# Kernel optimization log

Measured on AMD Instinct MI355X. Metric: run time of the kernel, lower is better.

Reference implementation:

```python
import jax, jax.numpy as jnp
import numpy as np

N, E, D, K = 32768, 16384, 4, 8          # nodes, hyperedges, edges/node, nodes/edge
IN_DIM, OUT_DIM, EDGE_DIM, NUM_HEADS = 128, 128, 64, 8


def setup_inputs() -> dict:
    key = jax.random.key(0)
    ks = jax.random.split(key, 16)
    s_in = 1.0 / np.sqrt(IN_DIM)
    s_out = 1.0 / np.sqrt(OUT_DIM)
    s_edge = 1.0 / np.sqrt(EDGE_DIM)
    return {
        "x": jax.random.normal(ks[0], (N, IN_DIM), jnp.float32),
        "edge_attr": jax.random.normal(ks[1], (E, EDGE_DIM), jnp.float32),
        "node_edges": jax.random.randint(ks[2], (N, D), 0, E),   # hyperedges containing each node
        "edge_nodes": jax.random.randint(ks[3], (E, K), 0, N),   # nodes inside each hyperedge
        "W_lin": jax.random.normal(ks[4], (OUT_DIM, IN_DIM), jnp.float32) * s_in,
        "W_edge": jax.random.normal(ks[5], (OUT_DIM, EDGE_DIM), jnp.float32) * s_edge,
        "Wq": jax.random.normal(ks[6], (OUT_DIM, OUT_DIM), jnp.float32) * s_out,
        "Wk": jax.random.normal(ks[7], (OUT_DIM, OUT_DIM), jnp.float32) * s_out,
        "Wv": jax.random.normal(ks[8], (OUT_DIM, OUT_DIM), jnp.float32) * s_out,
        "bq": jnp.zeros((OUT_DIM,), jnp.float32),
        "bk": jnp.zeros((OUT_DIM,), jnp.float32),
        "bv": jnp.zeros((OUT_DIM,), jnp.float32),
        "Wo": jax.random.normal(ks[9], (OUT_DIM, OUT_DIM), jnp.float32) * s_out,
        "bo": jnp.zeros((OUT_DIM,), jnp.float32),
    }


def reference(x, edge_attr, node_edges, edge_nodes,
              W_lin, W_edge, Wq, Wk, Wv, bq, bk, bv, Wo, bo):
    n, out_dim = x.shape[0], W_lin.shape[0]
    hd = out_dim // NUM_HEADS
    L = node_edges.shape[1] * edge_nodes.shape[1]  # D*K keys per node

    Wh = x @ W_lin.T                               # [N, out]
    We = edge_attr @ W_edge.T                      # [E, out]

    u_idx = edge_nodes[node_edges]                 # [N, D, K] neighbor node ids
    vals = Wh[u_idx]                               # [N, D, K, out]
    keys = vals + We[node_edges][:, :, None, :]    # key = Wh[u] + We[e]
    keys = keys.reshape(n, L, out_dim)
    vals = vals.reshape(n, L, out_dim)

    # torch nn.MultiheadAttention: single query per node (query = Wh[v])
    q = (Wh @ Wq.T + bq).reshape(n, NUM_HEADS, hd)
    k = (keys @ Wk.T + bk).reshape(n, L, NUM_HEADS, hd)
    v = (vals @ Wv.T + bv).reshape(n, L, NUM_HEADS, hd)

    scores = jnp.einsum('nhd,nlhd->nhl', q, k) / jnp.sqrt(jnp.asarray(hd, q.dtype))
    attn = jax.nn.softmax(scores, axis=-1)         # [N, H, L]
    ctx = jnp.einsum('nhl,nlhd->nhd', attn, v).reshape(n, out_dim)
    out = ctx @ Wo.T + bo
    return jax.nn.relu(out)
```

## Files before the change

### kernel.cpp

```cpp
#include <hip/hip_runtime.h>

#define N_NODES 32768
#define N_EDGES 16384
#define DEG 4
#define KPE 8
#define DIM 128
#define EDIM 64

typedef float f32x4 __attribute__((ext_vector_type(4)));
typedef __bf16 bf16x8 __attribute__((ext_vector_type(8)));
typedef __bf16 bf16x2 __attribute__((ext_vector_type(2)));
typedef unsigned short u16x8 __attribute__((ext_vector_type(8)));

static __device__ __forceinline__ unsigned short f2bf(float f) {
  union { float f; unsigned int u; } v; v.f = f;
  unsigned int r = (v.u + 0x7FFFu + ((v.u >> 16) & 1u)) >> 16;
  return (unsigned short)r;
}
static __device__ __forceinline__ float bflo(unsigned int v) {
  union { unsigned int u; float f; } x; x.u = v << 16; return x.f;
}
static __device__ __forceinline__ float bfhi(unsigned int v) {
  union { unsigned int u; float f; } x; x.u = v & 0xffff0000u; return x.f;
}

#if __has_builtin(__builtin_amdgcn_fdot2_f32_bf16)
static __device__ __forceinline__ float dot2bf(unsigned int a, unsigned int b, float c) {
  return __builtin_amdgcn_fdot2_f32_bf16(
      __builtin_bit_cast(bf16x2, a), __builtin_bit_cast(bf16x2, b), c, false);
}
#else
static __device__ __forceinline__ float dot2bf(unsigned int a, unsigned int b, float c) {
  c = fmaf(bflo(a), bflo(b), c);
  return fmaf(bfhi(a), bfhi(b), c);
}
#endif

__global__ __launch_bounds__(256) void wprep_kernel(
    const float* __restrict__ Wq, const float* __restrict__ Wk,
    const float* __restrict__ Wv, const float* __restrict__ Wlin,
    const float* __restrict__ Wedge, const float* __restrict__ Wo,
    unsigned short* __restrict__ CW, unsigned short* __restrict__ CWE,
    unsigned short* __restrict__ Wob)
{
  int id = blockIdx.x * 256 + threadIdx.x;
  if (id < 384 * 128) {
    int j = id >> 7, i = id & 127;
    const float* wrow; float scale = 1.0f;
    if (j < 128)      { wrow = Wq + j * 128; scale = 0.25f; }
    else if (j < 256) { wrow = Wk + (j - 128) * 128; }
    else              { wrow = Wv + (j - 256) * 128; }
    float s = 0.f;
    #pragma unroll 8
    for (int m = 0; m < 128; ++m) s += wrow[m] * Wlin[m * 128 + i];
    CW[id] = f2bf(s * scale);
  } else if (id < 384 * 128 + 128 * 64) {
    int id2 = id - 384 * 128; int j = id2 >> 6, t = id2 & 63;
    float s = 0.f;
    #pragma unroll 8
    for (int m = 0; m < 128; ++m) s += Wk[j * 128 + m] * Wedge[m * 64 + t];
    CWE[id2] = f2bf(s);
  } else if (id < 384 * 128 + 128 * 64 + 128 * 128) {
    int id3 = id - (384 * 128 + 128 * 64);
    Wob[id3] = f2bf(Wo[id3]);
  }
}

__global__ __launch_bounds__(256) void g1_kernel(
    const float* __restrict__ x, const unsigned short* __restrict__ CW,
    const float* __restrict__ bq, const float* __restrict__ bv,
    unsigned short* __restrict__ qb, unsigned short* __restrict__ Kb,
    unsigned short* __restrict__ Vb)
{
  const int wave = threadIdx.x >> 6, lane = threadIdx.x & 63;
  const int r16 = lane & 15, quad = lane >> 4;
  const int m0 = blockIdx.x * 64 + wave * 16;

  u16x8 av[4];
  const float* arow = x + (size_t)(m0 + r16) * DIM + quad * 8;
  #pragma unroll
  for (int kk = 0; kk < 4; ++kk) {
    float4 a0 = *(const float4*)(arow + kk * 32);
    float4 a1 = *(const float4*)(arow + kk * 32 + 4);
    u16x8 au;
    au[0] = f2bf(a0.x); au[1] = f2bf(a0.y); au[2] = f2bf(a0.z); au[3] = f2bf(a0.w);
    au[4] = f2bf(a1.x); au[5] = f2bf(a1.y); au[6] = f2bf(a1.z); au[7] = f2bf(a1.w);
    av[kk] = au;
  }

  #pragma unroll
  for (int g = 0; g < 6; ++g) {
    f32x4 acc[4];
    const f32x4 z = {0.f, 0.f, 0.f, 0.f};
    acc[0] = z; acc[1] = z; acc[2] = z; acc[3] = z;
    #pragma unroll
    for (int kk = 0; kk < 4; ++kk) {
      #pragma unroll
      for (int s = 0; s < 4; ++s) {
        u16x8 bu = *(const u16x8*)(CW + (size_t)(g * 64 + s * 16 + r16) * DIM + kk * 32 + quad * 8);
        acc[s] = __builtin_amdgcn_mfma_f32_16x16x32_bf16(
            __builtin_bit_cast(bf16x8, av[kk]), __builtin_bit_cast(bf16x8, bu), acc[s], 0, 0, 0);
      }
    }
    const int arr = g >> 1;
    const int colbase = (g & 1) * 64;
    unsigned short* dst = arr == 0 ? qb : (arr == 1 ? Kb : Vb);
    #pragma unroll
    for (int s = 0; s < 4; ++s) {
      int j = colbase + s * 16 + r16;
      float bias = arr == 0 ? 0.25f * bq[j] : (arr == 2 ? bv[j] : 0.f);
      #pragma unroll
      for (int r = 0; r < 4; ++r) {
        int m = m0 + quad * 4 + r;
        dst[(size_t)m * DIM + j] = f2bf(acc[s][r] + bias);
      }
    }
  }
}

__global__ __launch_bounds__(256) void g2_kernel(
    const float* __restrict__ ea, const unsigned short* __restrict__ CWE,
    const float* __restrict__ bk, unsigned short* __restrict__ WeKb)
{
  const int wave = threadIdx.x >> 6, lane = threadIdx.x & 63;
  const int r16 = lane & 15, quad = lane >> 4;
  const int m0 = blockIdx.x * 64 + wave * 16;
  const int n0 = blockIdx.y * 64;

  f32x4 acc[4];
  const f32x4 z = {0.f, 0.f, 0.f, 0.f};
  acc[0] = z; acc[1] = z; acc[2] = z; acc[3] = z;

  const float* arow = ea + (size_t)(m0 + r16) * EDIM + quad * 8;
  #pragma unroll
  for (int kk = 0; kk < 2; ++kk) {
    float4 a0 = *(const float4*)(arow + kk * 32);
    float4 a1 = *(const float4*)(arow + kk * 32 + 4);
    u16x8 au;
    au[0] = f2bf(a0.x); au[1] = f2bf(a0.y); au[2] = f2bf(a0.z); au[3] = f2bf(a0.w);
    au[4] = f2bf(a1.x); au[5] = f2bf(a1.y); au[6] = f2bf(a1.z); au[7] = f2bf(a1.w);
    bf16x8 av = __builtin_bit_cast(bf16x8, au);
    #pragma unroll
    for (int s = 0; s < 4; ++s) {
      u16x8 bu = *(const u16x8*)(CWE + (size_t)(n0 + s * 16 + r16) * EDIM + kk * 32 + quad * 8);
      acc[s] = __builtin_amdgcn_mfma_f32_16x16x32_bf16(
          av, __builtin_bit_cast(bf16x8, bu), acc[s], 0, 0, 0);
    }
  }

  #pragma unroll
  for (int s = 0; s < 4; ++s) {
    int j = n0 + s * 16 + r16;
    float bias = bk[j];
    #pragma unroll
    for (int r = 0; r < 4; ++r) {
      int m = m0 + quad * 4 + r;
      WeKb[(size_t)m * DIM + j] = f2bf(acc[s][r] + bias);
    }
  }
}

__global__ __launch_bounds__(256) void attn_kernel(
    const unsigned short* __restrict__ qb, const unsigned short* __restrict__ Kb,
    const unsigned short* __restrict__ Vb, const unsigned short* __restrict__ WeKb,
    const int* __restrict__ nedges, const int* __restrict__ enodes,
    unsigned short* __restrict__ ctxb)
{
  __shared__ __align__(16) float ldsP[4][288];
  const int wave = threadIdx.x >> 6, lane = threadIdx.x & 63;
  const int n = blockIdx.x * 4 + wave;
  const int l = lane & 31, half = lane >> 5;
  const int j = l >> 3, lo8 = l & 7;
  const int c0 = lane * 2;
  const int h = lane >> 3;

  int4 e4 = *(const int4*)(nedges + (size_t)n * DEG);
  int e = (j & 2) ? ((j & 1) ? e4.w : e4.z) : ((j & 1) ? e4.y : e4.x);
  int u = enodes[(size_t)e * KPE + lo8];

  int uu[32];
  *(int4*)&uu[0]  = *(const int4*)(enodes + (size_t)e4.x * KPE);
  *(int4*)&uu[4]  = *(const int4*)(enodes + (size_t)e4.x * KPE + 4);
  *(int4*)&uu[8]  = *(const int4*)(enodes + (size_t)e4.y * KPE);
  *(int4*)&uu[12] = *(const int4*)(enodes + (size_t)e4.y * KPE + 4);
  *(int4*)&uu[16] = *(const int4*)(enodes + (size_t)e4.z * KPE);
  *(int4*)&uu[20] = *(const int4*)(enodes + (size_t)e4.z * KPE + 4);
  *(int4*)&uu[24] = *(const int4*)(enodes + (size_t)e4.w * KPE);
  *(int4*)&uu[28] = *(const int4*)(enodes + (size_t)e4.w * KPE + 4);

  const uint4* qp = (const uint4*)(qb + (size_t)n * DIM + half * 64);
  const uint4* kp = (const uint4*)(Kb + (size_t)u * DIM + half * 64);
  const uint4* ep = (const uint4*)(WeKb + (size_t)e * DIM + half * 64);

  uint4 qv[8], kv[8], ev[8];
  #pragma unroll
  for (int ch = 0; ch < 8; ++ch) qv[ch] = qp[ch];
  #pragma unroll
  for (int ch = 0; ch < 8; ++ch) kv[ch] = kp[ch];
  #pragma unroll
  for (int ch = 0; ch < 8; ++ch) ev[ch] = ep[ch];

  unsigned int vv[32];
  #pragma unroll
  for (int t = 0; t < 32; ++t)
    vv[t] = *(const unsigned int*)(Vb + (size_t)uu[t] * DIM + c0);

  float s[4] = {0.f, 0.f, 0.f, 0.f};
  #pragma unroll
  for (int ch = 0; ch < 8; ++ch) {
    const int hi = ch >> 1;
    float t = s[hi];
    t = dot2bf(qv[ch].x, kv[ch].x, t); t = dot2bf(qv[ch].x, ev[ch].x, t);
    t = dot2bf(qv[ch].y, kv[ch].y, t); t = dot2bf(qv[ch].y, ev[ch].y, t);
    t = dot2bf(qv[ch].z, kv[ch].z, t); t = dot2bf(qv[ch].z, ev[ch].z, t);
    t = dot2bf(qv[ch].w, kv[ch].w, t); t = dot2bf(qv[ch].w, ev[ch].w, t);
    s[hi] = t;
  }

  #pragma unroll
  for (int hi = 0; hi < 4; ++hi) {
    float vmax = s[hi];
    #pragma unroll
    for (int off = 16; off >= 1; off >>= 1)
      vmax = fmaxf(vmax, __shfl_xor(vmax, off, 32));
    float ex = __expf(s[hi] - vmax);
    float sum = ex;
    #pragma unroll
    for (int off = 16; off >= 1; off >>= 1)
      sum += __shfl_xor(sum, off, 32);
    ldsP[wave][(half * 4 + hi) * 36 + l] = ex / sum;
  }
  __syncthreads();

  float a0 = 0.f, a1 = 0.f;
  #pragma unroll
  for (int t = 0; t < 8; ++t) {
    float4 p4 = *(const float4*)&ldsP[wave][h * 36 + t * 4];
    a0 = fmaf(p4.x, bflo(vv[t * 4 + 0]), a0); a1 = fmaf(p4.x, bfhi(vv[t * 4 + 0]), a1);
    a0 = fmaf(p4.y, bflo(vv[t * 4 + 1]), a0); a1 = fmaf(p4.y, bfhi(vv[t * 4 + 1]), a1);
    a0 = fmaf(p4.z, bflo(vv[t * 4 + 2]), a0); a1 = fmaf(p4.z, bfhi(vv[t * 4 + 2]), a1);
    a0 = fmaf(p4.w, bflo(vv[t * 4 + 3]), a0); a1 = fmaf(p4.w, bfhi(vv[t * 4 + 3]), a1);
  }
  unsigned int pk = (unsigned int)f2bf(a0) | ((unsigned int)f2bf(a1) << 16);
  *(unsigned int*)(ctxb + (size_t)n * DIM + c0) = pk;
}

__global__ __launch_bounds__(256) void g4_kernel(
    const unsigned short* __restrict__ ctxb, const unsigned short* __restrict__ Wob,
    const float* __restrict__ bo, float* __restrict__ out)
{
  const int wave = threadIdx.x >> 6, lane = threadIdx.x & 63;
  const int r16 = lane & 15, quad = lane >> 4;
  const int m0 = blockIdx.x * 64 + wave * 16;
  const int n0 = blockIdx.y * 64;

  f32x4 acc[4];
  const f32x4 z = {0.f, 0.f, 0.f, 0.f};
  acc[0] = z; acc[1] = z; acc[2] = z; acc[3] = z;

  #pragma unroll
  for (int kk = 0; kk < 4; ++kk) {
    u16x8 au = *(const u16x8*)(ctxb + (size_t)(m0 + r16) * DIM + kk * 32 + quad * 8);
    bf16x8 av = __builtin_bit_cast(bf16x8, au);
    #pragma unroll
    for (int s = 0; s < 4; ++s) {
      u16x8 bu = *(const u16x8*)(Wob + (size_t)(n0 + s * 16 + r16) * DIM + kk * 32 + quad * 8);
      acc[s] = __builtin_amdgcn_mfma_f32_16x16x32_bf16(
          av, __builtin_bit_cast(bf16x8, bu), acc[s], 0, 0, 0);
    }
  }

  #pragma unroll
  for (int s = 0; s < 4; ++s) {
    int j = n0 + s * 16 + r16;
    float bias = bo[j];
    #pragma unroll
    for (int r = 0; r < 4; ++r) {
      int m = m0 + quad * 4 + r;
      float v = acc[s][r] + bias;
      out[(size_t)m * DIM + j] = v > 0.f ? v : 0.f;
    }
  }
}

extern "C" void kernel_launch(void* const* d_in, const int* in_sizes, int n_in,
                              void* d_out, int out_size, void* d_ws, size_t ws_size,
                              hipStream_t stream)
{
  const float* x     = (const float*)d_in[0];
  const float* ea    = (const float*)d_in[1];
  const int* nedges  = (const int*)d_in[2];
  const int* enodes  = (const int*)d_in[3];
  const float* Wlin  = (const float*)d_in[4];
  const float* Wedge = (const float*)d_in[5];
  const float* Wq    = (const float*)d_in[6];
  const float* Wk    = (const float*)d_in[7];
  const float* Wv    = (const float*)d_in[8];
  const float* bq    = (const float*)d_in[9];
  const float* bk    = (const float*)d_in[10];
  const float* bv    = (const float*)d_in[11];
  const float* Wo    = (const float*)d_in[12];
  const float* bo    = (const float*)d_in[13];
  float* out = (float*)d_out;

  unsigned short* wsp = (unsigned short*)d_ws;
  unsigned short* CW   = wsp;  wsp += 384 * 128;
  unsigned short* CWE  = wsp;  wsp += 128 * 64;
  unsigned short* Wob  = wsp;  wsp += 128 * 128;
  unsigned short* qb   = wsp;  wsp += (size_t)N_NODES * DIM;
  unsigned short* Kb   = wsp;  wsp += (size_t)N_NODES * DIM;
  unsigned short* Vb   = wsp;  wsp += (size_t)N_NODES * DIM;
  unsigned short* WeKb = wsp;  wsp += (size_t)N_EDGES * DIM;
  unsigned short* ctxb = wsp;  wsp += (size_t)N_NODES * DIM;

  wprep_kernel<<<dim3(288), dim3(256), 0, stream>>>(Wq, Wk, Wv, Wlin, Wedge, Wo, CW, CWE, Wob);
  g1_kernel<<<dim3(512), dim3(256), 0, stream>>>(x, CW, bq, bv, qb, Kb, Vb);
  g2_kernel<<<dim3(256, 2), dim3(256), 0, stream>>>(ea, CWE, bk, WeKb);
  attn_kernel<<<dim3(8192), dim3(256), 0, stream>>>(qb, Kb, Vb, WeKb, nedges, enodes, ctxb);
  g4_kernel<<<dim3(512, 2), dim3(256), 0, stream>>>(ctxb, Wob, bo, out);
}
```

Measured before the change: 230.7 us.

## Stage V gathers into LDS via global_load_lds with one node per block

The attention kernel now launches one 64-thread block per node instead of four waves per 256-thread block. It gathers the 32 neighbour V rows directly into shared memory with global_load_lds rather than into 32 per-lane registers. The goal is to cut VGPR pressure and raise occupancy so more gather latency is hidden. In exchange it uses more LDS per block, adds many small blocks with higher launch overhead, and needs LDS reads in the weighted-sum loop.

```diff
diff --git a/kernel.cpp b/kernel.cpp
--- a/kernel.cpp
+++ b/kernel.cpp
@@ -11,6 +11,7 @@
 typedef __bf16 bf16x8 __attribute__((ext_vector_type(8)));
 typedef __bf16 bf16x2 __attribute__((ext_vector_type(2)));
 typedef unsigned short u16x8 __attribute__((ext_vector_type(8)));
+typedef unsigned int u32;
 
 static __device__ __forceinline__ unsigned short f2bf(float f) {
   union { float f; unsigned int u; } v; v.f = f;
@@ -160,15 +161,16 @@
   }
 }
 
-__global__ __launch_bounds__(256) void attn_kernel(
+__global__ __launch_bounds__(64, 2) void attn_kernel(
     const unsigned short* __restrict__ qb, const unsigned short* __restrict__ Kb,
     const unsigned short* __restrict__ Vb, const unsigned short* __restrict__ WeKb,
     const int* __restrict__ nedges, const int* __restrict__ enodes,
     unsigned short* __restrict__ ctxb)
 {
-  __shared__ __align__(16) float ldsP[4][288];
-  const int wave = threadIdx.x >> 6, lane = threadIdx.x & 63;
-  const int n = blockIdx.x * 4 + wave;
+  __shared__ __align__(16) unsigned short ldsV[32][128];
+  __shared__ __align__(16) float ldsP[8][36];
+  const int lane = threadIdx.x;
+  const int n = blockIdx.x;
   const int l = lane & 31, half = lane >> 5;
   const int j = l >> 3, lo8 = l & 7;
   const int c0 = lane * 2;
@@ -178,20 +180,18 @@
   int e = (j & 2) ? ((j & 1) ? e4.w : e4.z) : ((j & 1) ? e4.y : e4.x);
   int u = enodes[(size_t)e * KPE + lo8];
 
-  int uu[32];
-  *(int4*)&uu[0]  = *(const int4*)(enodes + (size_t)e4.x * KPE);
-  *(int4*)&uu[4]  = *(const int4*)(enodes + (size_t)e4.x * KPE + 4);
-  *(int4*)&uu[8]  = *(const int4*)(enodes + (size_t)e4.y * KPE);
-  *(int4*)&uu[12] = *(const int4*)(enodes + (size_t)e4.y * KPE + 4);
-  *(int4*)&uu[16] = *(const int4*)(enodes + (size_t)e4.z * KPE);
-  *(int4*)&uu[20] = *(const int4*)(enodes + (size_t)e4.z * KPE + 4);
-  *(int4*)&uu[24] = *(const int4*)(enodes + (size_t)e4.w * KPE);
-  *(int4*)&uu[28] = *(const int4*)(enodes + (size_t)e4.w * KPE + 4);
+  int4 m0 = *(const int4*)(enodes + (size_t)e4.x * KPE);
+  int4 m1 = *(const int4*)(enodes + (size_t)e4.x * KPE + 4);
+  int4 m2 = *(const int4*)(enodes + (size_t)e4.y * KPE);
+  int4 m3 = *(const int4*)(enodes + (size_t)e4.y * KPE + 4);
+  int4 m4 = *(const int4*)(enodes + (size_t)e4.z * KPE);
+  int4 m5 = *(const int4*)(enodes + (size_t)e4.z * KPE + 4);
+  int4 m6 = *(const int4*)(enodes + (size_t)e4.w * KPE);
+  int4 m7 = *(const int4*)(enodes + (size_t)e4.w * KPE + 4);
 
   const uint4* qp = (const uint4*)(qb + (size_t)n * DIM + half * 64);
   const uint4* kp = (const uint4*)(Kb + (size_t)u * DIM + half * 64);
   const uint4* ep = (const uint4*)(WeKb + (size_t)e * DIM + half * 64);
-
   uint4 qv[8], kv[8], ev[8];
   #pragma unroll
   for (int ch = 0; ch < 8; ++ch) qv[ch] = qp[ch];
@@ -200,10 +200,21 @@
   #pragma unroll
   for (int ch = 0; ch < 8; ++ch) ev[ch] = ep[ch];
 
-  unsigned int vv[32];
-  #pragma unroll
-  for (int t = 0; t < 32; ++t)
-    vv[t] = *(const unsigned int*)(Vb + (size_t)uu[t] * DIM + c0);
+#define STAGE_V(t, node) do {                                                   \
+    const u32* gp_ = (const u32*)(Vb + (size_t)(node) * DIM) + lane;            \
+    __builtin_amdgcn_global_load_lds(                                           \
+        (const __attribute__((address_space(1))) u32*)gp_,                      \
+        (__attribute__((address_space(3))) u32*)&ldsV[t][0], 4, 0, 0);          \
+  } while (0)
+  STAGE_V(0,  m0.x); STAGE_V(1,  m0.y); STAGE_V(2,  m0.z); STAGE_V(3,  m0.w);
+  STAGE_V(4,  m1.x); STAGE_V(5,  m1.y); STAGE_V(6,  m1.z); STAGE_V(7,  m1.w);
+  STAGE_V(8,  m2.x); STAGE_V(9,  m2.y); STAGE_V(10, m2.z); STAGE_V(11, m2.w);
+  STAGE_V(12, m3.x); STAGE_V(13, m3.y); STAGE_V(14, m3.z); STAGE_V(15, m3.w);
+  STAGE_V(16, m4.x); STAGE_V(17, m4.y); STAGE_V(18, m4.z); STAGE_V(19, m4.w);
+  STAGE_V(20, m5.x); STAGE_V(21, m5.y); STAGE_V(22, m5.z); STAGE_V(23, m5.w);
+  STAGE_V(24, m6.x); STAGE_V(25, m6.y); STAGE_V(26, m6.z); STAGE_V(27, m6.w);
+  STAGE_V(28, m7.x); STAGE_V(29, m7.y); STAGE_V(30, m7.z); STAGE_V(31, m7.w);
+#undef STAGE_V
 
   float s[4] = {0.f, 0.f, 0.f, 0.f};
   #pragma unroll
@@ -228,18 +239,22 @@
     #pragma unroll
     for (int off = 16; off >= 1; off >>= 1)
       sum += __shfl_xor(sum, off, 32);
-    ldsP[wave][(half * 4 + hi) * 36 + l] = ex / sum;
+    ldsP[half * 4 + hi][l] = ex / sum;
   }
   __syncthreads();
 
   float a0 = 0.f, a1 = 0.f;
   #pragma unroll
   for (int t = 0; t < 8; ++t) {
-    float4 p4 = *(const float4*)&ldsP[wave][h * 36 + t * 4];
-    a0 = fmaf(p4.x, bflo(vv[t * 4 + 0]), a0); a1 = fmaf(p4.x, bfhi(vv[t * 4 + 0]), a1);
-    a0 = fmaf(p4.y, bflo(vv[t * 4 + 1]), a0); a1 = fmaf(p4.y, bfhi(vv[t * 4 + 1]), a1);
-    a0 = fmaf(p4.z, bflo(vv[t * 4 + 2]), a0); a1 = fmaf(p4.z, bfhi(vv[t * 4 + 2]), a1);
-    a0 = fmaf(p4.w, bflo(vv[t * 4 + 3]), a0); a1 = fmaf(p4.w, bfhi(vv[t * 4 + 3]), a1);
+    float4 p4 = *(const float4*)&ldsP[h][t * 4];
+    u32 v0 = *(const u32*)&ldsV[t * 4 + 0][c0];
+    u32 v1 = *(const u32*)&ldsV[t * 4 + 1][c0];
+    u32 v2 = *(const u32*)&ldsV[t * 4 + 2][c0];
+    u32 v3 = *(const u32*)&ldsV[t * 4 + 3][c0];
+    a0 = fmaf(p4.x, bflo(v0), a0); a1 = fmaf(p4.x, bfhi(v0), a1);
+    a0 = fmaf(p4.y, bflo(v1), a0); a1 = fmaf(p4.y, bfhi(v1), a1);
+    a0 = fmaf(p4.z, bflo(v2), a0); a1 = fmaf(p4.z, bfhi(v2), a1);
+    a0 = fmaf(p4.w, bflo(v3), a0); a1 = fmaf(p4.w, bfhi(v3), a1);
   }
   unsigned int pk = (unsigned int)f2bf(a0) | ((unsigned int)f2bf(a1) << 16);
   *(unsigned int*)(ctxb + (size_t)n * DIM + c0) = pk;
@@ -316,6 +331,6 @@
   wprep_kernel<<<dim3(288), dim3(256), 0, stream>>>(Wq, Wk, Wv, Wlin, Wedge, Wo, CW, CWE, Wob);
   g1_kernel<<<dim3(512), dim3(256), 0, stream>>>(x, CW, bq, bv, qb, Kb, Vb);
   g2_kernel<<<dim3(256, 2), dim3(256), 0, stream>>>(ea, CWE, bk, WeKb);
-  attn_kernel<<<dim3(8192), dim3(256), 0, stream>>>(qb, Kb, Vb, WeKb, nedges, enodes, ctxb);
+  attn_kernel<<<dim3(32768), dim3(64), 0, stream>>>(qb, Kb, Vb, WeKb, nedges, enodes, ctxb);
   g4_kernel<<<dim3(512, 2), dim3(256), 0, stream>>>(ctxb, Wob, bo, out);
 }
```

Result: faster. 215.5 us (-6.6%).

## Pipeline attention gathers via global_load_lds double buffering and merge projection kernels

Applied to the files above, without the earlier changes.

The attention kernel now runs one wave per block, processing 8 nodes each, and stages each node's gathered K, V, edge-key and query rows into LDS with direct global-to-LDS loads. Buffers are double-buffered so the next node's gathers are in flight while the current node's scores and context are computed, with hand-written vmcnt waits. The node and edge projection GEMMs are merged into one launch to save a kernel launch. The hard-coded waitcnt counts are fragile and depend on how many loads the compiler emits, and the large LDS footprint limits occupancy.

```diff
diff --git a/kernel.cpp b/kernel.cpp
--- a/kernel.cpp
+++ b/kernel.cpp
@@ -11,6 +11,7 @@
 typedef __bf16 bf16x8 __attribute__((ext_vector_type(8)));
 typedef __bf16 bf16x2 __attribute__((ext_vector_type(2)));
 typedef unsigned short u16x8 __attribute__((ext_vector_type(8)));
+typedef unsigned int u32;
 
 static __device__ __forceinline__ unsigned short f2bf(float f) {
   union { float f; unsigned int u; } v; v.f = f;
@@ -66,183 +67,244 @@
   }
 }
 
-__global__ __launch_bounds__(256) void g1_kernel(
+__global__ __launch_bounds__(256) void g12_kernel(
     const float* __restrict__ x, const unsigned short* __restrict__ CW,
     const float* __restrict__ bq, const float* __restrict__ bv,
     unsigned short* __restrict__ qb, unsigned short* __restrict__ Kb,
-    unsigned short* __restrict__ Vb)
+    unsigned short* __restrict__ Vb,
+    const float* __restrict__ ea, const unsigned short* __restrict__ CWE,
+    const float* __restrict__ bk, unsigned short* __restrict__ WeKb)
 {
   const int wave = threadIdx.x >> 6, lane = threadIdx.x & 63;
   const int r16 = lane & 15, quad = lane >> 4;
-  const int m0 = blockIdx.x * 64 + wave * 16;
-
-  u16x8 av[4];
-  const float* arow = x + (size_t)(m0 + r16) * DIM + quad * 8;
-  #pragma unroll
-  for (int kk = 0; kk < 4; ++kk) {
-    float4 a0 = *(const float4*)(arow + kk * 32);
-    float4 a1 = *(const float4*)(arow + kk * 32 + 4);
-    u16x8 au;
-    au[0] = f2bf(a0.x); au[1] = f2bf(a0.y); au[2] = f2bf(a0.z); au[3] = f2bf(a0.w);
-    au[4] = f2bf(a1.x); au[5] = f2bf(a1.y); au[6] = f2bf(a1.z); au[7] = f2bf(a1.w);
-    av[kk] = au;
-  }
-
-  #pragma unroll
-  for (int g = 0; g < 6; ++g) {
+
+  if (blockIdx.x < 512) {
+    const int m0 = blockIdx.x * 64 + wave * 16;
+    u16x8 av[4];
+    const float* arow = x + (size_t)(m0 + r16) * DIM + quad * 8;
+    #pragma unroll
+    for (int kk = 0; kk < 4; ++kk) {
+      float4 a0 = *(const float4*)(arow + kk * 32);
+      float4 a1 = *(const float4*)(arow + kk * 32 + 4);
+      u16x8 au;
+      au[0] = f2bf(a0.x); au[1] = f2bf(a0.y); au[2] = f2bf(a0.z); au[3] = f2bf(a0.w);
+      au[4] = f2bf(a1.x); au[5] = f2bf(a1.y); au[6] = f2bf(a1.z); au[7] = f2bf(a1.w);
+      av[kk] = au;
+    }
+    #pragma unroll
+    for (int g = 0; g < 6; ++g) {
+      f32x4 acc[4];
+      const f32x4 z = {0.f, 0.f, 0.f, 0.f};
+      acc[0] = z; acc[1] = z; acc[2] = z; acc[3] = z;
+      #pragma unroll
+      for (int kk = 0; kk < 4; ++kk) {
+        #pragma unroll
+        for (int s = 0; s < 4; ++s) {
+          u16x8 bu = *(const u16x8*)(CW + (size_t)(g * 64 + s * 16 + r16) * DIM + kk * 32 + quad * 8);
+          acc[s] = __builtin_amdgcn_mfma_f32_16x16x32_bf16(
+              __builtin_bit_cast(bf16x8, av[kk]), __builtin_bit_cast(bf16x8, bu), acc[s], 0, 0, 0);
+        }
+      }
+      const int arr = g >> 1;
+      const int colbase = (g & 1) * 64;
+      unsigned short* dst = arr == 0 ? qb : (arr == 1 ? Kb : Vb);
+      #pragma unroll
+      for (int s = 0; s < 4; ++s) {
+        int j = colbase + s * 16 + r16;
+        float bias = arr == 0 ? 0.25f * bq[j] : (arr == 2 ? bv[j] : 0.f);
+        #pragma unroll
+        for (int r = 0; r < 4; ++r) {
+          int m = m0 + quad * 4 + r;
+          dst[(size_t)m * DIM + j] = f2bf(acc[s][r] + bias);
+        }
+      }
+    }
+  } else {
+    const int idx = blockIdx.x - 512;
+    const int m0 = (idx >> 1) * 64 + wave * 16;
+    const int n0 = (idx & 1) * 64;
     f32x4 acc[4];
     const f32x4 z = {0.f, 0.f, 0.f, 0.f};
     acc[0] = z; acc[1] = z; acc[2] = z; acc[3] = z;
-    #pragma unroll
-    for (int kk = 0; kk < 4; ++kk) {
+    const float* arow = ea + (size_t)(m0 + r16) * EDIM + quad * 8;
+    #pragma unroll
+    for (int kk = 0; kk < 2; ++kk) {
+      float4 a0 = *(const float4*)(arow + kk * 32);
+      float4 a1 = *(const float4*)(arow + kk * 32 + 4);
+      u16x8 au;
+      au[0] = f2bf(a0.x); au[1] = f2bf(a0.y); au[2] = f2bf(a0.z); au[3] = f2bf(a0.w);
+      au[4] = f2bf(a1.x); au[5] = f2bf(a1.y); au[6] = f2bf(a1.z); au[7] = f2bf(a1.w);
+      bf16x8 av = __builtin_bit_cast(bf16x8, au);
       #pragma unroll
       for (int s = 0; s < 4; ++s) {
-        u16x8 bu = *(const u16x8*)(CW + (size_t)(g * 64 + s * 16 + r16) * DIM + kk * 32 + quad * 8);
+        u16x8 bu = *(const u16x8*)(CWE + (size_t)(n0 + s * 16 + r16) * EDIM + kk * 32 + quad * 8);
         acc[s] = __builtin_amdgcn_mfma_f32_16x16x32_bf16(
-            __builtin_bit_cast(bf16x8, av[kk]), __builtin_bit_cast(bf16x8, bu), acc[s], 0, 0, 0);
+            av, __builtin_bit_cast(bf16x8, bu), acc[s], 0, 0, 0);
       }
     }
-    const int arr = g >> 1;
-    const int colbase = (g & 1) * 64;
-    unsigned short* dst = arr == 0 ? qb : (arr == 1 ? Kb : Vb);
     #pragma unroll
     for (int s = 0; s < 4; ++s) {
-      int j = colbase + s * 16 + r16;
-      float bias = arr == 0 ? 0.25f * bq[j] : (arr == 2 ? bv[j] : 0.f);
+      int j = n0 + s * 16 + r16;
+      float bias = bk[j];
       #pragma unroll
       for (int r = 0; r < 4; ++r) {
         int m = m0 + quad * 4 + r;
-        dst[(size_t)m * DIM + j] = f2bf(acc[s][r] + bias);
+        WeKb[(size_t)m * DIM + j] = f2bf(acc[s][r] + bias);
       }
     }
   }
 }
 
-__global__ __launch_bounds__(256) void g2_kernel(
-    const float* __restrict__ ea, const unsigned short* __restrict__ CWE,
-    const float* __restrict__ bk, unsigned short* __restrict__ WeKb)
-{
-  const int wave = threadIdx.x >> 6, lane = threadIdx.x & 63;
-  const int r16 = lane & 15, quad = lane >> 4;
-  const int m0 = blockIdx.x * 64 + wave * 16;
-  const int n0 = blockIdx.y * 64;
-
-  f32x4 acc[4];
-  const f32x4 z = {0.f, 0.f, 0.f, 0.f};
-  acc[0] = z; acc[1] = z; acc[2] = z; acc[3] = z;
-
-  const float* arow = ea + (size_t)(m0 + r16) * EDIM + quad * 8;
-  #pragma unroll
-  for (int kk = 0; kk < 2; ++kk) {
-    float4 a0 = *(const float4*)(arow + kk * 32);
-    float4 a1 = *(const float4*)(arow + kk * 32 + 4);
-    u16x8 au;
-    au[0] = f2bf(a0.x); au[1] = f2bf(a0.y); au[2] = f2bf(a0.z); au[3] = f2bf(a0.w);
-    au[4] = f2bf(a1.x); au[5] = f2bf(a1.y); au[6] = f2bf(a1.z); au[7] = f2bf(a1.w);
-    bf16x8 av = __builtin_bit_cast(bf16x8, au);
-    #pragma unroll
-    for (int s = 0; s < 4; ++s) {
-      u16x8 bu = *(const u16x8*)(CWE + (size_t)(n0 + s * 16 + r16) * EDIM + kk * 32 + quad * 8);
-      acc[s] = __builtin_amdgcn_mfma_f32_16x16x32_bf16(
-          av, __builtin_bit_cast(bf16x8, bu), acc[s], 0, 0, 0);
-    }
-  }
-
-  #pragma unroll
-  for (int s = 0; s < 4; ++s) {
-    int j = n0 + s * 16 + r16;
-    float bias = bk[j];
-    #pragma unroll
-    for (int r = 0; r < 4; ++r) {
-      int m = m0 + quad * 4 + r;
-      WeKb[(size_t)m * DIM + j] = f2bf(acc[s][r] + bias);
-    }
-  }
-}
-
-__global__ __launch_bounds__(256) void attn_kernel(
+#define OFF_V 0
+#define OFF_K 8192
+#define OFF_E 16896
+#define OFF_Q 17984
+#define BUFSZ 18256
+#define OFF_P 36512
+
+struct IdxPack { int4 e4, m0, m1, m2, m3, m4, m5, m6, m7; };
+
+static __device__ __forceinline__ IdxPack load_idx(
+    const int* __restrict__ ne, const int* __restrict__ en, int n) {
+  IdxPack I;
+  I.e4 = *(const int4*)(ne + (size_t)n * DEG);
+  I.m0 = *(const int4*)(en + (size_t)I.e4.x * KPE);
+  I.m1 = *(const int4*)(en + (size_t)I.e4.x * KPE + 4);
+  I.m2 = *(const int4*)(en + (size_t)I.e4.y * KPE);
+  I.m3 = *(const int4*)(en + (size_t)I.e4.y * KPE + 4);
+  I.m4 = *(const int4*)(en + (size_t)I.e4.z * KPE);
+  I.m5 = *(const int4*)(en + (size_t)I.e4.z * KPE + 4);
+  I.m6 = *(const int4*)(en + (size_t)I.e4.w * KPE);
+  I.m7 = *(const int4*)(en + (size_t)I.e4.w * KPE + 4);
+  return I;
+}
+
+#define GLDS(gp, ldsp, sz) __builtin_amdgcn_global_load_lds(               \
+    (const __attribute__((address_space(1))) u32*)(gp),                    \
+    (__attribute__((address_space(3))) u32*)(ldsp), sz, 0, 0)
+
+static __device__ __forceinline__ void stage_node(
+    unsigned char* buf, const IdxPack& I,
+    const unsigned short* __restrict__ Kb, const unsigned short* __restrict__ Vb,
+    const unsigned short* __restrict__ WeKb, const unsigned short* __restrict__ qb,
+    int n, int lane)
+{
+  int4 mm[8] = {I.m0, I.m1, I.m2, I.m3, I.m4, I.m5, I.m6, I.m7};
+  #pragma unroll
+  for (int t = 0; t < 8; ++t) {
+    GLDS((const u32*)(Kb + (size_t)mm[t].x * DIM) + lane, buf + OFF_K + (t*4+0)*272, 4);
+    GLDS((const u32*)(Kb + (size_t)mm[t].y * DIM) + lane, buf + OFF_K + (t*4+1)*272, 4);
+    GLDS((const u32*)(Kb + (size_t)mm[t].z * DIM) + lane, buf + OFF_K + (t*4+2)*272, 4);
+    GLDS((const u32*)(Kb + (size_t)mm[t].w * DIM) + lane, buf + OFF_K + (t*4+3)*272, 4);
+  }
+  GLDS((const u32*)(WeKb + (size_t)I.e4.x * DIM) + lane, buf + OFF_E + 0*272, 4);
+  GLDS((const u32*)(WeKb + (size_t)I.e4.y * DIM) + lane, buf + OFF_E + 1*272, 4);
+  GLDS((const u32*)(WeKb + (size_t)I.e4.z * DIM) + lane, buf + OFF_E + 2*272, 4);
+  GLDS((const u32*)(WeKb + (size_t)I.e4.w * DIM) + lane, buf + OFF_E + 3*272, 4);
+  GLDS((const u32*)(qb + (size_t)n * DIM) + lane, buf + OFF_Q, 4);
+  const int vr = lane >> 4, vc = lane & 15;
+  #pragma unroll
+  for (int t = 0; t < 8; ++t) {
+    int row = (vr & 2) ? ((vr & 1) ? mm[t].w : mm[t].z)
+                       : ((vr & 1) ? mm[t].y : mm[t].x);
+    GLDS((const u32*)(Vb + (size_t)row * DIM) + vc * 4, buf + OFF_V + t * 1024, 16);
+  }
+}
+
+static __device__ __forceinline__ void scores_softmax(
+    const unsigned char* buf, float* ldsP, int lane)
+{
+  const int l = lane & 31, half = lane >> 5;
+  const unsigned char* krow = buf + OFF_K + l * 272 + half * 128;
+  const unsigned char* erow = buf + OFF_E + (l >> 3) * 272 + half * 128;
+  const unsigned char* qrow = buf + OFF_Q + half * 128;
+  float s[4] = {0.f, 0.f, 0.f, 0.f};
+  #pragma unroll
+  for (int ch = 0; ch < 8; ++ch) {
+    uint4 qc = *(const uint4*)(qrow + ch * 16);
+    uint4 kc = *(const uint4*)(krow + ch * 16);
+    uint4 ec = *(const uint4*)(erow + ch * 16);
+    const int hi = ch >> 1;
+    float t = s[hi];
+    t = dot2bf(qc.x, kc.x, t); t = dot2bf(qc.x, ec.x, t);
+    t = dot2bf(qc.y, kc.y, t); t = dot2bf(qc.y, ec.y, t);
+    t = dot2bf(qc.z, kc.z, t); t = dot2bf(qc.z, ec.z, t);
+    t = dot2bf(qc.w, kc.w, t); t = dot2bf(qc.w, ec.w, t);
+    s[hi] = t;
+  }
+  #pragma unroll
+  for (int hi = 0; hi < 4; ++hi) {
+    float vmax = s[hi];
+    #pragma unroll
+    for (int off = 16; off >= 1; off >>= 1)
+      vmax = fmaxf(vmax, __shfl_xor(vmax, off, 32));
+    float ex = __expf(s[hi] - vmax);
+    float sum = ex;
+    #pragma unroll
+    for (int off = 16; off >= 1; off >>= 1)
+      sum += __shfl_xor(sum, off, 32);
+    ldsP[(half * 4 + hi) * 36 + l] = ex / sum;
+  }
+}
+
+static __device__ __forceinline__ void ctx_store(
+    const unsigned char* buf, const float* ldsP, int lane,
+    unsigned short* __restrict__ ctxb, int n)
+{
+  const int h = lane >> 3;
+  const int c0 = lane * 2;
+  float a0 = 0.f, a1 = 0.f;
+  #pragma unroll
+  for (int t = 0; t < 8; ++t) {
+    float4 p4 = *(const float4*)(ldsP + h * 36 + t * 4);
+    u32 v0 = *(const u32*)(buf + OFF_V + (t * 4 + 0) * 256 + lane * 4);
+    u32 v1 = *(const u32*)(buf + OFF_V + (t * 4 + 1) * 256 + lane * 4);
+    u32 v2 = *(const u32*)(buf + OFF_V + (t * 4 + 2) * 256 + lane * 4);
+    u32 v3 = *(const u32*)(buf + OFF_V + (t * 4 + 3) * 256 + lane * 4);
+    a0 = fmaf(p4.x, bflo(v0), a0); a1 = fmaf(p4.x, bfhi(v0), a1);
+    a0 = fmaf(p4.y, bflo(v1), a0); a1 = fmaf(p4.y, bfhi(v1), a1);
+    a0 = fmaf(p4.z, bflo(v2), a0); a1 = fmaf(p4.z, bfhi(v2), a1);
+    a0 = fmaf(p4.w, bflo(v3), a0); a1 = fmaf(p4.w, bfhi(v3), a1);
+  }
+  unsigned int pk = (unsigned int)f2bf(a0) | ((unsigned int)f2bf(a1) << 16);
+  __builtin_nontemporal_store(pk, (u32*)(ctxb + (size_t)n * DIM + c0));
+}
+
+__global__ __launch_bounds__(64, 2) void attn_kernel(
     const unsigned short* __restrict__ qb, const unsigned short* __restrict__ Kb,
     const unsigned short* __restrict__ Vb, const unsigned short* __restrict__ WeKb,
     const int* __restrict__ nedges, const int* __restrict__ enodes,
     unsigned short* __restrict__ ctxb)
 {
-  __shared__ __align__(16) float ldsP[4][288];
-  const int wave = threadIdx.x >> 6, lane = threadIdx.x & 63;
-  const int n = blockIdx.x * 4 + wave;
-  const int l = lane & 31, half = lane >> 5;
-  const int j = l >> 3, lo8 = l & 7;
-  const int c0 = lane * 2;
-  const int h = lane >> 3;
-
-  int4 e4 = *(const int4*)(nedges + (size_t)n * DEG);
-  int e = (j & 2) ? ((j & 1) ? e4.w : e4.z) : ((j & 1) ? e4.y : e4.x);
-  int u = enodes[(size_t)e * KPE + lo8];
-
-  int uu[32];
-  *(int4*)&uu[0]  = *(const int4*)(enodes + (size_t)e4.x * KPE);
-  *(int4*)&uu[4]  = *(const int4*)(enodes + (size_t)e4.x * KPE + 4);
-  *(int4*)&uu[8]  = *(const int4*)(enodes + (size_t)e4.y * KPE);
-  *(int4*)&uu[12] = *(const int4*)(enodes + (size_t)e4.y * KPE + 4);
-  *(int4*)&uu[16] = *(const int4*)(enodes + (size_t)e4.z * KPE);
-  *(int4*)&uu[20] = *(const int4*)(enodes + (size_t)e4.z * KPE + 4);
-  *(int4*)&uu[24] = *(const int4*)(enodes + (size_t)e4.w * KPE);
-  *(int4*)&uu[28] = *(const int4*)(enodes + (size_t)e4.w * KPE + 4);
-
-  const uint4* qp = (const uint4*)(qb + (size_t)n * DIM + half * 64);
-  const uint4* kp = (const uint4*)(Kb + (size_t)u * DIM + half * 64);
-  const uint4* ep = (const uint4*)(WeKb + (size_t)e * DIM + half * 64);
-
-  uint4 qv[8], kv[8], ev[8];
-  #pragma unroll
-  for (int ch = 0; ch < 8; ++ch) qv[ch] = qp[ch];
-  #pragma unroll
-  for (int ch = 0; ch < 8; ++ch) kv[ch] = kp[ch];
-  #pragma unroll
-  for (int ch = 0; ch < 8; ++ch) ev[ch] = ep[ch];
-
-  unsigned int vv[32];
-  #pragma unroll
-  for (int t = 0; t < 32; ++t)
-    vv[t] = *(const unsigned int*)(Vb + (size_t)uu[t] * DIM + c0);
-
-  float s[4] = {0.f, 0.f, 0.f, 0.f};
-  #pragma unroll
-  for (int ch = 0; ch < 8; ++ch) {
-    const int hi = ch >> 1;
-    float t = s[hi];
-    t = dot2bf(qv[ch].x, kv[ch].x, t); t = dot2bf(qv[ch].x, ev[ch].x, t);
-    t = dot2bf(qv[ch].y, kv[ch].y, t); t = dot2bf(qv[ch].y, ev[ch].y, t);
-    t = dot2bf(qv[ch].z, kv[ch].z, t); t = dot2bf(qv[ch].z, ev[ch].z, t);
-    t = dot2bf(qv[ch].w, kv[ch].w, t); t = dot2bf(qv[ch].w, ev[ch].w, t);
-    s[hi] = t;
-  }
-
-  #pragma unroll
-  for (int hi = 0; hi < 4; ++hi) {
-    float vmax = s[hi];
-    #pragma unroll
-    for (int off = 16; off >= 1; off >>= 1)
-      vmax = fmaxf(vmax, __shfl_xor(vmax, off, 32));
-    float ex = __expf(s[hi] - vmax);
-    float sum = ex;
-    #pragma unroll
-    for (int off = 16; off >= 1; off >>= 1)
-      sum += __shfl_xor(sum, off, 32);
-    ldsP[wave][(half * 4 + hi) * 36 + l] = ex / sum;
-  }
-  __syncthreads();
-
-  float a0 = 0.f, a1 = 0.f;
-  #pragma unroll
-  for (int t = 0; t < 8; ++t) {
-    float4 p4 = *(const float4*)&ldsP[wave][h * 36 + t * 4];
-    a0 = fmaf(p4.x, bflo(vv[t * 4 + 0]), a0); a1 = fmaf(p4.x, bfhi(vv[t * 4 + 0]), a1);
-    a0 = fmaf(p4.y, bflo(vv[t * 4 + 1]), a0); a1 = fmaf(p4.y, bfhi(vv[t * 4 + 1]), a1);
-    a0 = fmaf(p4.z, bflo(vv[t * 4 + 2]), a0); a1 = fmaf(p4.z, bfhi(vv[t * 4 + 2]), a1);
-    a0 = fmaf(p4.w, bflo(vv[t * 4 + 3]), a0); a1 = fmaf(p4.w, bfhi(vv[t * 4 + 3]), a1);
-  }
-  unsigned int pk = (unsigned int)f2bf(a0) | ((unsigned int)f2bf(a1) << 16);
-  *(unsigned int*)(ctxb + (size_t)n * DIM + c0) = pk;
+  __shared__ __align__(16) unsigned char slds[37664];
+  const int lane = threadIdx.x;
+  const int n0 = blockIdx.x * 8;
+  float* ldsP = (float*)(slds + OFF_P);
+
+  IdxPack ia = load_idx(nedges, enodes, n0 + 0);
+  IdxPack ib = load_idx(nedges, enodes, n0 + 1);
+  stage_node(slds, ia, Kb, Vb, WeKb, qb, n0 + 0, lane);
+
+#define STEP(kk, IA, IB, HAS2, HAS1, W1, W2)                                   \
+  {                                                                            \
+    if (HAS2) IA = load_idx(nedges, enodes, n0 + kk + 2);                      \
+    if (HAS1) stage_node(slds + ((kk + 1) & 1) * BUFSZ, IB, Kb, Vb, WeKb, qb,  \
+                         n0 + kk + 1, lane);                                   \
+    asm volatile("s_waitcnt vmcnt(" W1 ")" ::: "memory");                      \
+    scores_softmax(slds + ((kk) & 1) * BUFSZ, ldsP, lane);                     \
+    asm volatile("s_waitcnt vmcnt(" W2 ")" ::: "memory");                      \
+    ctx_store(slds + ((kk) & 1) * BUFSZ, ldsP, lane, ctxb, n0 + kk);           \
+  }
+
+  STEP(0, ia, ib, 1, 1, "53", "45")
+  STEP(1, ib, ia, 1, 1, "54", "46")
+  STEP(2, ia, ib, 1, 1, "54", "46")
+  STEP(3, ib, ia, 1, 1, "54", "46")
+  STEP(4, ia, ib, 1, 1, "54", "46")
+  STEP(5, ib, ia, 1, 1, "54", "46")
+  STEP(6, ia, ib, 0, 1, "54", "46")
+  STEP(7, ib, ia, 0, 0, "9",  "1")
+#undef STEP
 }
 
 __global__ __launch_bounds__(256) void g4_kernel(
@@ -314,8 +376,7 @@
   unsigned short* ctxb = wsp;  wsp += (size_t)N_NODES * DIM;
 
   wprep_kernel<<<dim3(288), dim3(256), 0, stream>>>(Wq, Wk, Wv, Wlin, Wedge, Wo, CW, CWE, Wob);
-  g1_kernel<<<dim3(512), dim3(256), 0, stream>>>(x, CW, bq, bv, qb, Kb, Vb);
-  g2_kernel<<<dim3(256, 2), dim3(256), 0, stream>>>(ea, CWE, bk, WeKb);
-  attn_kernel<<<dim3(8192), dim3(256), 0, stream>>>(qb, Kb, Vb, WeKb, nedges, enodes, ctxb);
+  g12_kernel<<<dim3(1024), dim3(256), 0, stream>>>(x, CW, bq, bv, qb, Kb, Vb, ea, CWE, bk, WeKb);
+  attn_kernel<<<dim3(4096), dim3(64), 0, stream>>>(qb, Kb, Vb, WeKb, nedges, enodes, ctxb);
   g4_kernel<<<dim3(512, 2), dim3(256), 0, stream>>>(ctxb, Wob, bo, out);
 }
```

After: 286.3 us. 24.1% more time.
